# Performance work log

Measured on AMD Instinct MI355X. Metric: run time of the kernel, lower is better.

The kernel has to match this reference:

```python
import jax, jax.numpy as jnp
import numpy as np

_L, _DEPTH, _M, _NGEN, _C = 4, 7, 256, 8, 16


def _build_tree():
    # Complete _L-ary tree in BFS (level) order. t columns: [label, parent, position, child_0.._L-1]
    rng = np.random.default_rng(0)
    sizes = [_L ** d for d in range(_DEPTH + 1)]
    t_limits = np.concatenate([[0], np.cumsum(sizes)]).astype(np.int32)
    n = int(t_limits[-1])
    u = np.arange(n)
    parent = np.where(u > 0, (u - 1) // _L, 0)
    pos = np.where(u > 0, (u - 1) % _L, 0)
    labels = rng.integers(0, _M, n)
    ch = _L * u[:, None] + 1 + np.arange(_L)[None, :]
    ch = np.where(ch < n, ch, 0)  # 0 == no child (root is never a child)
    t = np.concatenate([labels[:, None], parent[:, None], pos[:, None], ch], axis=1).astype(np.int32)
    return t, t_limits


def setup_inputs():
    key = jax.random.key(0)
    ka, kb, kp = jax.random.split(key, 3)
    t, t_limits = _build_tree()
    return {
        'a': jax.random.normal(ka, (_NGEN, _C, _C, _L), jnp.float32),
        'b': jax.random.normal(kb, (_NGEN, _C, _M), jnp.float32),
        'pi': jax.random.normal(kp, (_NGEN, _C), jnp.float32),
        't': jnp.asarray(t),
        't_limits': jnp.asarray(t_limits),
    }


def _htmm_likelihood(a, b, pi, t, t_limits):
    t = np.asarray(t)
    lim = np.asarray(t_limits)
    n_levels = len(lim) - 1
    n = int(lim[-1])
    n_gen, C, _, L = a.shape
    sm_a = jax.nn.softmax(a, axis=1)    # [G, Ci(child), Cj(parent), L]
    sm_b = jax.nn.softmax(b, axis=2)    # [G, C, M]
    sm_pi = jax.nn.softmax(pi, axis=1)  # [G, C]

    # ---- preliminary downward: per-node state priors, level by level ----
    prior = jnp.zeros((n_gen, n, C), sm_pi.dtype).at[:, 0, :].set(sm_pi)
    for lev in range(1, n_levels):
        lo, hi = int(lim[lev]), int(lim[lev + 1])
        pos, pa = t[lo:hi, 2], t[lo:hi, 1]
        a_pos = sm_a[:, :, :, pos]                        # [G, Ci, Cj, nl]
        lev_prior = jnp.einsum('gijn,gnj->gni', a_pos, prior[:, pa, :])
        prior = prior.at[:, lo:hi, :].set(lev_prior)

    # ---- upward pass ----
    beta_i = jnp.zeros((n_gen, n, C), sm_pi.dtype)
    beta_il = jnp.zeros((n_gen, n + 1, C), sm_pi.dtype)   # extra dummy slot for padded children
    lo, hi = int(lim[-2]), int(lim[-1])                   # leaves
    em = sm_b[:, :, t[lo:hi, 0]].transpose(0, 2, 1)       # [G, n_leaf, C]
    bl = em * prior[:, lo:hi, :]
    beta_i = beta_i.at[:, lo:hi, :].set(bl / bl.sum(2, keepdims=True))
    a_t = sm_a.transpose(0, 3, 1, 2)                      # [G, L(pos), Ci, Cj]
    for lev in range(n_levels - 2, -1, -1):
        lo, hi = int(lim[lev]), int(lim[lev + 1])
        ch = t[lo:hi, 3:]                                 # [nl, L]
        mask = ch > 0
        safe = np.where(mask, ch, 0)
        ratio = beta_i[:, safe, :] / prior[:, safe, :]    # [G, nl, L, C]
        bil = jnp.einsum('gnlc,glcp->gnlp', ratio, a_t)   # [G, nl, L, Cj]
        aux = jnp.prod(jnp.where(mask[None, :, :, None], bil, 1.0), axis=2)
        em = sm_b[:, :, t[lo:hi, 0]].transpose(0, 2, 1)
        bi = aux * em * prior[:, lo:hi, :]
        beta_i = beta_i.at[:, lo:hi, :].set(bi / bi.sum(2, keepdims=True))
        scat = np.where(mask, ch, n).reshape(-1)          # padded children go to dummy slot
        beta_il = beta_il.at[:, scat, :].set(bil.reshape(n_gen, -1, C))
    beta_il = beta_il[:, :n, :].at[:, 0, :].set(0.0)

    # ---- downward pass: smoothed posteriors ----
    eps_i = jnp.zeros((n_gen, n, C), sm_pi.dtype).at[:, 0, :].set(beta_i[:, 0, :])
    eps_ijl = jnp.zeros((n_gen, n, C, C), sm_pi.dtype)
    for lev in range(1, n_levels):
        lo, hi = int(lim[lev]), int(lim[lev + 1])
        pos, pa = t[lo:hi, 2], t[lo:hi, 1]
        a_pos = sm_a[:, :, :, pos].transpose(0, 3, 1, 2)  # [G, nl, Ci, Cj]
        num = beta_i[:, lo:hi, :, None] * a_pos * eps_i[:, pa, None, :]
        den = prior[:, lo:hi, :, None] * beta_il[:, lo:hi, None, :]
        e_ijl = num / den
        e_i = e_ijl.sum(3)
        e_i = e_i / e_i.sum(2, keepdims=True)
        eps_i = eps_i.at[:, lo:hi, :].set(e_i)
        eps_ijl = eps_ijl.at[:, lo:hi, :, :].set(e_ijl)

    # ---- log-likelihood ----
    pi_lh = jnp.sum(eps_i[:, 0, :] * jnp.log(sm_pi), axis=-1)
    b_nodes = sm_b[:, :, t[:, 0]].transpose(0, 2, 1)      # [G, n, C]
    b_lh = jnp.sum(eps_i * jnp.log(b_nodes), axis=(1, 2))
    a_pos_all = sm_a[:, :, :, t[1:, 2]].transpose(0, 3, 1, 2)
    a_lh = jnp.sum(eps_ijl[:, 1:] * jnp.log(a_pos_all), axis=(1, 2, 3))
    return pi_lh + b_lh + a_lh  # [n_gen]


def reference(a, b, pi, t, t_limits):
    return _htmm_likelihood(a, b, pi, t, t_limits)
```

## Files before the change

### kernel.cpp

```cpp
#include <hip/hip_runtime.h>

#define NGEN 8
#define NC 16
#define NM 256
#define NNODE 21845

#define OFF_SMA_T  ((size_t)0)
#define OFF_SALA   ((size_t)8192)
#define OFF_SMA_U  ((size_t)16384)
#define OFF_SMB_T  ((size_t)24576)
#define OFF_LSMB_T ((size_t)57344)
#define OFF_SMPI   ((size_t)90112)
#define OFF_LSMPI  ((size_t)90240)
#define OFF_LAB    ((size_t)90368)
#define OFF_R4     ((size_t)112224)
#define OFF_EPS4   ((size_t)144992)
#define OFF_ST     ((size_t)177760)
#define ST_R7   0
#define ST_R6   1024
#define ST_R5   1280
#define ST_BIL7 1344
#define ST_BIL6 2368
#define ST_BIL5 2624
#define ST_SZ   2688

__device__ __forceinline__ float red16(float v) {
    v += __shfl_xor(v, 1, 16);
    v += __shfl_xor(v, 2, 16);
    v += __shfl_xor(v, 4, 16);
    v += __shfl_xor(v, 8, 16);
    return v;
}
__device__ __forceinline__ float rcpf(float x) { return __builtin_amdgcn_rcpf(x); }

__device__ __forceinline__ float dot16(const float* A, const float* row) {
    const float4* r4 = (const float4*)row;
    float s = 0.f;
#pragma unroll
    for (int q = 0; q < 4; ++q) {
        float4 t = r4[q];
        s += A[4 * q] * t.x + A[4 * q + 1] * t.y + A[4 * q + 2] * t.z + A[4 * q + 3] * t.w;
    }
    return s;
}
__device__ __forceinline__ void dot16x2(const float* A, const float* B, const float* row,
                                        float& s1, float& s2) {
    const float4* r4 = (const float4*)row;
#pragma unroll
    for (int q = 0; q < 4; ++q) {
        float4 t = r4[q];
        s1 += A[4 * q] * t.x + A[4 * q + 1] * t.y + A[4 * q + 2] * t.z + A[4 * q + 3] * t.w;
        s2 += B[4 * q] * t.x + B[4 * q + 1] * t.y + B[4 * q + 2] * t.z + B[4 * q + 3] * t.w;
    }
}

__device__ __forceinline__ void up_step4(const float (*Rch)[16], float (*BILch)[16],
                                         const float (*Ppar)[16], float (*Rpar)[16],
                                         const float* smb, int lab, int nd, int l, int p,
                                         const float* Aup) {
    int ch = 4 * nd + l;
    float bil = dot16(Aup, Rch[ch]);
    BILch[ch][p] = bil;
    float t0 = bil * __shfl_xor(bil, 16);
    float aux = t0 * __shfl_xor(t0, 32);
    float q0 = aux * smb[(size_t)lab * 16 + p];
    float bi = q0 * Ppar[nd][p];
    float ssum = red16(bi);
    if (l == 0) Rpar[nd][p] = q0 * rcpf(ssum);
}

__global__ __launch_bounds__(128) void k_init(const float* __restrict__ a,
                                              const float* __restrict__ b,
                                              const float* __restrict__ pi,
                                              const int* __restrict__ t,
                                              float* __restrict__ ws, float* __restrict__ out) {
    int bx = blockIdx.x, tid = threadIdx.x;
    if (bx < 128) {
        for (int k = bx * 128 + tid; k < NNODE; k += 128 * 128)
            ((int*)(ws + OFF_LAB))[k] = t[k * 7];
        if (tid < 64) {
            int g = bx >> 4, i = bx & 15;
            float v[4];
            float mx = -1e30f;
#pragma unroll
            for (int q = 0; q < 4; ++q) {
                v[q] = b[((size_t)(g * NC + i)) * NM + tid + 64 * q];
                mx = fmaxf(mx, v[q]);
            }
#pragma unroll
            for (int o = 1; o < 64; o <<= 1) mx = fmaxf(mx, __shfl_xor(mx, o));
            float e[4], s = 0.f;
#pragma unroll
            for (int q = 0; q < 4; ++q) { e[q] = expf(v[q] - mx); s += e[q]; }
#pragma unroll
            for (int o = 1; o < 64; o <<= 1) s += __shfl_xor(s, o);
            float ls = logf(s), rs = 1.0f / s;
#pragma unroll
            for (int q = 0; q < 4; ++q) {
                int m = tid + 64 * q;
                ws[OFF_SMB_T + ((size_t)g * NM + m) * NC + i] = e[q] * rs;
                ws[OFF_LSMB_T + ((size_t)g * NM + m) * NC + i] = v[q] - mx - ls;
            }
        }
        return;
    }
    int g = bx - 128;
    if (tid < 64) {
        int j = tid >> 2, l = tid & 3;
        size_t base = ((size_t)(g * NC) * NC + j) * 4 + l;
        float v[16];
        float mx = -1e30f;
#pragma unroll
        for (int i = 0; i < 16; ++i) { v[i] = a[base + (size_t)i * 64]; mx = fmaxf(mx, v[i]); }
        float e[16], s = 0.0f;
#pragma unroll
        for (int i = 0; i < 16; ++i) { e[i] = expf(v[i] - mx); s += e[i]; }
        float ls = logf(s), rs = 1.0f / s;
        size_t tb = ((size_t)(g * NC + j) * 4 + l) * NC;
#pragma unroll
        for (int i = 0; i < 16; ++i) {
            float sm = e[i] * rs;
            float lg = v[i] - mx - ls;
            ws[OFF_SMA_T + tb + i] = sm;
            ws[OFF_SALA + tb + i] = sm * lg;
            ws[OFF_SMA_U + ((size_t)(g * NC + i) * 4 + l) * NC + j] = sm;
        }
    } else if (tid == 64) {
        float v[16];
        float mx = -1e30f;
#pragma unroll
        for (int i = 0; i < 16; ++i) { v[i] = pi[g * NC + i]; mx = fmaxf(mx, v[i]); }
        float e[16], s = 0.0f;
#pragma unroll
        for (int i = 0; i < 16; ++i) { e[i] = expf(v[i] - mx); s += e[i]; }
        float ls = logf(s), rs = 1.0f / s;
#pragma unroll
        for (int i = 0; i < 16; ++i) {
            ws[OFF_SMPI + g * NC + i] = e[i] * rs;
            ws[OFF_LSMPI + g * NC + i] = v[i] - mx - ls;
        }
        out[g] = 0.0f;
    }
}

__global__ __launch_bounds__(256) void k_sub_up(float* __restrict__ ws) {
    int s = blockIdx.x, g = blockIdx.y, tid = threadIdx.x;
    int v = 85 + s;
    int i = tid & 15, grp = tid >> 4, pos = grp & 3;
    int lane = tid & 63, wv = tid >> 6;
    int l = lane >> 4, p = lane & 15;
    const float* sAg = ws + OFF_SMA_T + (size_t)g * 1024;
    const float* Aug = ws + OFF_SMA_U + (size_t)g * 1024;
    const float* smb = ws + OFF_SMB_T + (size_t)g * 4096;
    const int* LAB = (const int*)(ws + OFF_LAB);

    __shared__ __align__(16) float ST[ST_SZ];
    float (*R7)[16]   = (float(*)[16])(ST + ST_R7);
    float (*R6)[16]   = (float(*)[16])(ST + ST_R6);
    float (*R5)[16]   = (float(*)[16])(ST + ST_R5);
    float (*BIL7)[16] = (float(*)[16])(ST + ST_BIL7);
    float (*BIL6)[16] = (float(*)[16])(ST + ST_BIL6);
    float (*BIL5)[16] = (float(*)[16])(ST + ST_BIL5);
    __shared__ __align__(16) float P5[4][16], P6[16][16];
    __shared__ __align__(16) float P4[16];
    __shared__ int labs[85];

    if (tid < 64) labs[21 + tid] = LAB[64 * v + 21 + tid];
    else if (tid < 80) labs[5 + (tid - 64)] = LAB[16 * v + 5 + (tid - 64)];
    else if (tid < 84) labs[1 + (tid - 80)] = LAB[4 * v + 1 + (tid - 80)];
    else if (tid == 84) labs[0] = LAB[v];
    else if (tid >= 128 && tid < 144) {
        int v3 = (v - 1) >> 2, v2 = (v3 - 1) >> 2, v1 = (v2 - 1) >> 2;
        int chain[4] = {v1, v2, v3, v};
        float pr = ws[OFF_SMPI + g * 16 + i];
#pragma unroll
        for (int k = 0; k < 4; ++k) {
            int pk = (chain[k] - 1) & 3;
            float sacc = 0.f;
#pragma unroll
            for (int j = 0; j < 16; ++j) sacc += sAg[(j * 4 + pk) * 16 + i] * __shfl(pr, j, 16);
            pr = sacc;
        }
        P4[i] = pr;
    }
    float Areg[16];
#pragma unroll
    for (int j = 0; j < 16; ++j) Areg[j] = sAg[(j * 4 + pos) * 16 + i];
    __syncthreads();

    if (tid < 64) P5[grp][i] = dot16(Areg, P4);
    __syncthreads();
    P6[grp][i] = dot16(Areg, P5[grp >> 2]);
    __syncthreads();
#pragma unroll
    for (int k = 0; k < 4; ++k) {
        int nl = grp + 16 * k;
        float s7 = dot16(Areg, P6[nl >> 2]);
        float smbv = smb[(size_t)labs[21 + nl] * 16 + i];
        float bl = smbv * s7;
        float ssum = red16(bl);
        R7[nl][i] = smbv * rcpf(ssum);
    }
    __syncthreads();
    float Aup[16];
#pragma unroll
    for (int c = 0; c < 16; ++c) Aup[c] = Aug[(c * 4 + l) * 16 + p];
#pragma unroll
    for (int r = 0; r < 4; ++r)
        up_step4(R7, BIL7, P6, R6, smb, labs[5 + (wv + 4 * r)], wv + 4 * r, l, p, Aup);
    __syncthreads();
    up_step4(R6, BIL6, P5, R5, smb, labs[1 + wv], wv, l, p, Aup);
    __syncthreads();
    if (wv == 0) {
        float bil = dot16(Aup, R5[l]);
        BIL5[l][p] = bil;
        float t0 = bil * __shfl_xor(bil, 16);
        float aux = t0 * __shfl_xor(t0, 32);
        float q0 = aux * smb[(size_t)labs[0] * 16 + p];
        float bi = q0 * P4[p];
        float ssum = red16(bi);
        if (l == 0) ws[OFF_R4 + ((size_t)g * 256 + s) * 16 + p] = q0 * rcpf(ssum);
    }
    __syncthreads();
    float* dst = ws + OFF_ST + (size_t)(g * 256 + s) * ST_SZ;
#pragma unroll
    for (int k = tid; k < ST_SZ / 4; k += 256)
        ((float4*)dst)[k] = ((const float4*)ST)[k];
}

__global__ __launch_bounds__(1024) void k_top(float* __restrict__ ws, float* __restrict__ out) {
    int g = blockIdx.x, tid = threadIdx.x;
    int i = tid & 15, grp = tid >> 4, pos = grp & 3;
    int lane = tid & 63, wv = tid >> 6;
    int l = lane >> 4, p = lane & 15;
    const float* sAg = ws + OFF_SMA_T + (size_t)g * 1024;
    const float* sLg = ws + OFF_SALA + (size_t)g * 1024;
    const float* Aug = ws + OFF_SMA_U + (size_t)g * 1024;
    const float* smb = ws + OFF_SMB_T + (size_t)g * 4096;
    const float* lsmb = ws + OFF_LSMB_T + (size_t)g * 4096;
    const float* r4g = ws + OFF_R4 + (size_t)g * 4096;
    float* eps4 = ws + OFF_EPS4 + (size_t)g * 4096;
    const int* LAB = (const int*)(ws + OFF_LAB);

    __shared__ float Pt[85][16], Bt[85][16], BILt[341][16];
    __shared__ int labt[341];
    __shared__ float wsum[16];

    float Areg[16], Aup[16], sLreg[16];
#pragma unroll
    for (int j = 0; j < 16; ++j) {
        Areg[j] = sAg[(j * 4 + pos) * 16 + i];
        sLreg[j] = sLg[(j * 4 + pos) * 16 + i];
    }
#pragma unroll
    for (int c = 0; c < 16; ++c) Aup[c] = Aug[(c * 4 + l) * 16 + p];
    if (tid < 341) labt[tid] = LAB[tid];
    if (tid < 16) Pt[0][i] = ws[OFF_SMPI + g * 16 + i];
    __syncthreads();
    if (grp < 4) {
        float pv = Pt[0][i];
        float s = 0.f;
#pragma unroll
        for (int j = 0; j < 16; ++j) s += Areg[j] * __shfl(pv, j, 16);
        Pt[1 + grp][i] = s;
    }
    __syncthreads();
    if (grp < 16) {
        float pv = Pt[1 + (grp >> 2)][i];
        float s = 0.f;
#pragma unroll
        for (int j = 0; j < 16; ++j) s += Areg[j] * __shfl(pv, j, 16);
        Pt[5 + grp][i] = s;
    }
    __syncthreads();
    {
        float pv = Pt[5 + (grp >> 2)][i];
        float s = 0.f;
#pragma unroll
        for (int j = 0; j < 16; ++j) s += Areg[j] * __shfl(pv, j, 16);
        Pt[21 + grp][i] = s;
    }
    __syncthreads();
    for (int r = 0; r < 4; ++r) {
        int nd = wv + 16 * r;
        int chl = 4 * nd + l;
        float rv = r4g[(size_t)chl * 16 + p];
        float bil = 0.f;
#pragma unroll
        for (int c = 0; c < 16; ++c) bil += __shfl(rv, c, 16) * Aup[c];
        BILt[85 + chl][p] = bil;
        float t0 = bil * __shfl_xor(bil, 16);
        float aux = t0 * __shfl_xor(t0, 32);
        float bi = aux * smb[(size_t)labt[21 + nd] * 16 + p] * Pt[21 + nd][p];
        float ssum = red16(bi);
        if (l == 0) Bt[21 + nd][p] = bi * rcpf(ssum);
    }
    __syncthreads();
    {
        int nd = wv, ch = 21 + 4 * nd + l;
        float rv = Bt[ch][p] * rcpf(Pt[ch][p]);
        float bil = 0.f;
#pragma unroll
        for (int c = 0; c < 16; ++c) bil += __shfl(rv, c, 16) * Aup[c];
        BILt[ch][p] = bil;
        float t0 = bil * __shfl_xor(bil, 16);
        float aux = t0 * __shfl_xor(t0, 32);
        float bi = aux * smb[(size_t)labt[5 + nd] * 16 + p] * Pt[5 + nd][p];
        float ssum = red16(bi);
        if (l == 0) Bt[5 + nd][p] = bi * rcpf(ssum);
    }
    __syncthreads();
    if (wv < 4) {
        int nd = wv, ch = 5 + 4 * nd + l;
        float rv = Bt[ch][p] * rcpf(Pt[ch][p]);
        float bil = 0.f;
#pragma unroll
        for (int c = 0; c < 16; ++c) bil += __shfl(rv, c, 16) * Aup[c];
        BILt[ch][p] = bil;
        float t0 = bil * __shfl_xor(bil, 16);
        float aux = t0 * __shfl_xor(t0, 32);
        float bi = aux * smb[(size_t)labt[1 + nd] * 16 + p] * Pt[1 + nd][p];
        float ssum = red16(bi);
        if (l == 0) Bt[1 + nd][p] = bi * rcpf(ssum);
    }
    __syncthreads();
    if (wv == 0) {
        int ch = 1 + l;
        float rv = Bt[ch][p] * rcpf(Pt[ch][p]);
        float bil = 0.f;
#pragma unroll
        for (int c = 0; c < 16; ++c) bil += __shfl(rv, c, 16) * Aup[c];
        BILt[ch][p] = bil;
        float t0 = bil * __shfl_xor(bil, 16);
        float aux = t0 * __shfl_xor(t0, 32);
        float bi = aux * smb[(size_t)labt[0] * 16 + p] * Pt[0][p];
        float ssum = red16(bi);
        if (l == 0) Bt[0][p] = bi * rcpf(ssum);
    }
    __syncthreads();
    float acc = 0.f;
    if (tid < 16)
        acc += Bt[0][i] * (ws[OFF_LSMPI + g * 16 + i] + lsmb[(size_t)labt[0] * 16 + i]);
    if (grp < 4) {
        int row = 1 + grp;
        float w = Bt[0][i] * rcpf(BILt[row][i]);
        float c0 = Bt[row][i] * rcpf(Pt[row][i]);
        float s1 = 0.f, s2 = 0.f;
#pragma unroll
        for (int j = 0; j < 16; ++j) { float wj = __shfl(w, j, 16); s1 += Areg[j] * wj; s2 += sLreg[j] * wj; }
        float esum = c0 * s1, tot = red16(esum), ev = esum * rcpf(tot);
        Bt[row][i] = ev;
        acc += c0 * s2 + ev * lsmb[(size_t)labt[row] * 16 + i];
    }
    __syncthreads();
    if (grp < 16) {
        int row = 5 + grp, pa = 1 + (grp >> 2);
        float w = Bt[pa][i] * rcpf(BILt[row][i]);
        float c0 = Bt[row][i] * rcpf(Pt[row][i]);
        float s1 = 0.f, s2 = 0.f;
#pragma unroll
        for (int j = 0; j < 16; ++j) { float wj = __shfl(w, j, 16); s1 += Areg[j] * wj; s2 += sLreg[j] * wj; }
        float esum = c0 * s1, tot = red16(esum), ev = esum * rcpf(tot);
        Bt[row][i] = ev;
        acc += c0 * s2 + ev * lsmb[(size_t)labt[row] * 16 + i];
    }
    __syncthreads();
    {
        int row = 21 + grp, pa = 5 + (grp >> 2);
        float w = Bt[pa][i] * rcpf(BILt[row][i]);
        float c0 = Bt[row][i] * rcpf(Pt[row][i]);
        float s1 = 0.f, s2 = 0.f;
#pragma unroll
        for (int j = 0; j < 16; ++j) { float wj = __shfl(w, j, 16); s1 += Areg[j] * wj; s2 += sLreg[j] * wj; }
        float esum = c0 * s1, tot = red16(esum), ev = esum * rcpf(tot);
        Bt[row][i] = ev;
        acc += c0 * s2 + ev * lsmb[(size_t)labt[row] * 16 + i];
    }
    __syncthreads();
    for (int k = 0; k < 4; ++k) {
        int nl = grp + 64 * k;
        int row = 85 + nl, pa = 21 + (nl >> 2);
        float w = Bt[pa][i] * rcpf(BILt[row][i]);
        float c0 = r4g[(size_t)nl * 16 + i];
        float s1 = 0.f, s2 = 0.f;
#pragma unroll
        for (int j = 0; j < 16; ++j) { float wj = __shfl(w, j, 16); s1 += Areg[j] * wj; s2 += sLreg[j] * wj; }
        float esum = c0 * s1, tot = red16(esum), ev = esum * rcpf(tot);
        eps4[(size_t)nl * 16 + i] = ev;
        acc += c0 * s2 + ev * lsmb[(size_t)labt[row] * 16 + i];
    }
#pragma unroll
    for (int o = 1; o < 64; o <<= 1) acc += __shfl_xor(acc, o);
    if ((tid & 63) == 0) wsum[tid >> 6] = acc;
    __syncthreads();
    if (tid == 0) {
        float stot = 0.f;
#pragma unroll
        for (int w2 = 0; w2 < 16; ++w2) stot += wsum[w2];
        atomicAdd(&out[g], stot);
    }
}

__global__ __launch_bounds__(256) void k_sub_down(float* __restrict__ ws, float* __restrict__ out) {
    int s = blockIdx.x, g = blockIdx.y, tid = threadIdx.x;
    int v = 85 + s;
    int i = tid & 15, grp = tid >> 4, pos = grp & 3;
    const float* sAg = ws + OFF_SMA_T + (size_t)g * 1024;
    const float* sLg = ws + OFF_SALA + (size_t)g * 1024;
    const float* lsmb = ws + OFF_LSMB_T + (size_t)g * 4096;
    const int* LAB = (const int*)(ws + OFF_LAB);

    __shared__ __align__(16) float ST[ST_SZ];
    float (*R7)[16]   = (float(*)[16])(ST + ST_R7);
    float (*R6)[16]   = (float(*)[16])(ST + ST_R6);
    float (*R5)[16]   = (float(*)[16])(ST + ST_R5);
    float (*BIL7)[16] = (float(*)[16])(ST + ST_BIL7);
    float (*BIL6)[16] = (float(*)[16])(ST + ST_BIL6);
    float (*BIL5)[16] = (float(*)[16])(ST + ST_BIL5);
    __shared__ __align__(16) float E4[16];
    __shared__ int labs[85];
    __shared__ float wsum[4];

    const float* src = ws + OFF_ST + (size_t)(g * 256 + s) * ST_SZ;
#pragma unroll
    for (int k = tid; k < ST_SZ / 4; k += 256)
        ((float4*)ST)[k] = ((const float4*)src)[k];
    if (tid < 64) labs[21 + tid] = LAB[64 * v + 21 + tid];
    else if (tid < 80) labs[5 + (tid - 64)] = LAB[16 * v + 5 + (tid - 64)];
    else if (tid < 84) labs[1 + (tid - 80)] = LAB[4 * v + 1 + (tid - 80)];
    else if (tid == 84) labs[0] = LAB[v];
    else if (tid >= 96 && tid < 112) E4[tid - 96] = ws[OFF_EPS4 + ((size_t)g * 256 + s) * 16 + (tid - 96)];

    float Areg[16], sLreg[16];
#pragma unroll
    for (int j = 0; j < 16; ++j) {
        Areg[j] = sAg[(j * 4 + pos) * 16 + i];
        sLreg[j] = sLg[(j * 4 + pos) * 16 + i];
    }
    __syncthreads();

    float acc = 0.f;
    if (tid < 64) {
        float w = E4[i] * rcpf(BIL5[grp][i]);
        BIL5[grp][i] = w;
        float c0 = R5[grp][i];
        float s1 = 0.f, s2 = 0.f;
        dot16x2(Areg, sLreg, BIL5[grp], s1, s2);
        float esum = c0 * s1, tot = red16(esum), ev = esum * rcpf(tot);
        R5[grp][i] = ev;
        acc += c0 * s2 + ev * lsmb[(size_t)labs[1 + grp] * 16 + i];
    }
    __syncthreads();
    {
        float w = R5[grp >> 2][i] * rcpf(BIL6[grp][i]);
        BIL6[grp][i] = w;
        float c0 = R6[grp][i];
        float s1 = 0.f, s2 = 0.f;
        dot16x2(Areg, sLreg, BIL6[grp], s1, s2);
        float esum = c0 * s1, tot = red16(esum), ev = esum * rcpf(tot);
        R6[grp][i] = ev;
        acc += c0 * s2 + ev * lsmb[(size_t)labs[5 + grp] * 16 + i];
    }
    __syncthreads();
#pragma unroll
    for (int k = 0; k < 4; ++k) {
        int nl = grp + 16 * k;
        float w = R6[nl >> 2][i] * rcpf(BIL7[nl][i]);
        BIL7[nl][i] = w;
        float c0 = R7[nl][i];
        float s1 = 0.f, s2 = 0.f;
        dot16x2(Areg, sLreg, BIL7[nl], s1, s2);
        float esum = c0 * s1, tot = red16(esum), ev = esum * rcpf(tot);
        acc += c0 * s2 + ev * lsmb[(size_t)labs[21 + nl] * 16 + i];
    }
#pragma unroll
    for (int o = 1; o < 64; o <<= 1) acc += __shfl_xor(acc, o);
    if ((tid & 63) == 0) wsum[tid >> 6] = acc;
    __syncthreads();
    if (tid == 0) atomicAdd(&out[g], wsum[0] + wsum[1] + wsum[2] + wsum[3]);
}

extern "C" void kernel_launch(void* const* d_in, const int* in_sizes, int n_in,
                              void* d_out, int out_size, void* d_ws, size_t ws_size,
                              hipStream_t stream) {
    const float* a = (const float*)d_in[0];
    const float* b = (const float*)d_in[1];
    const float* pi = (const float*)d_in[2];
    const int* t = (const int*)d_in[3];
    float* out = (float*)d_out;
    float* ws = (float*)d_ws;

    k_init<<<136, 128, 0, stream>>>(a, b, pi, t, ws, out);
    k_sub_up<<<dim3(256, NGEN), 256, 0, stream>>>(ws);
    k_top<<<NGEN, 1024, 0, stream>>>(ws, out);
    k_sub_down<<<dim3(256, NGEN), 256, 0, stream>>>(ws, out);
}
```

Measured before the change: 76.08 us.

## Read labels directly from tree, use DPP reductions and LDS dot products

Drops the label-compaction pass in the init kernel and has each kernel read labels with a strided gather straight from the tree array. The 16-lane shuffle reductions become DPP row operations. In the top kernel, the shuffle-broadcast matrix-vector products are replaced by dot products that read vectors from shared memory, with the intermediate weights written back to LDS first. These changes trim instruction count and a global write/read pass, at the cost of uncoalesced strided label loads.

New measurement: 65.87 us. -13.4%, faster.

```diff
diff --git a/kernel.cpp b/kernel.cpp
--- a/kernel.cpp
+++ b/kernel.cpp
@@ -12,7 +12,6 @@
 #define OFF_LSMB_T ((size_t)57344)
 #define OFF_SMPI   ((size_t)90112)
 #define OFF_LSMPI  ((size_t)90240)
-#define OFF_LAB    ((size_t)90368)
 #define OFF_R4     ((size_t)112224)
 #define OFF_EPS4   ((size_t)144992)
 #define OFF_ST     ((size_t)177760)
@@ -24,11 +23,16 @@
 #define ST_BIL5 2624
 #define ST_SZ   2688
 
+template <int CTRL>
+__device__ __forceinline__ float dpp_row_add(float v) {
+    int s = __builtin_amdgcn_update_dpp(0, __float_as_int(v), CTRL, 0xf, 0xf, false);
+    return v + __int_as_float(s);
+}
 __device__ __forceinline__ float red16(float v) {
-    v += __shfl_xor(v, 1, 16);
-    v += __shfl_xor(v, 2, 16);
-    v += __shfl_xor(v, 4, 16);
-    v += __shfl_xor(v, 8, 16);
+    v = dpp_row_add<0x121>(v);
+    v = dpp_row_add<0x122>(v);
+    v = dpp_row_add<0x124>(v);
+    v = dpp_row_add<0x128>(v);
     return v;
 }
 __device__ __forceinline__ float rcpf(float x) { return __builtin_amdgcn_rcpf(x); }
@@ -72,12 +76,9 @@
 __global__ __launch_bounds__(128) void k_init(const float* __restrict__ a,
                                               const float* __restrict__ b,
                                               const float* __restrict__ pi,
-                                              const int* __restrict__ t,
                                               float* __restrict__ ws, float* __restrict__ out) {
     int bx = blockIdx.x, tid = threadIdx.x;
     if (bx < 128) {
-        for (int k = bx * 128 + tid; k < NNODE; k += 128 * 128)
-            ((int*)(ws + OFF_LAB))[k] = t[k * 7];
         if (tid < 64) {
             int g = bx >> 4, i = bx & 15;
             float v[4];
@@ -143,7 +144,7 @@
     }
 }
 
-__global__ __launch_bounds__(256) void k_sub_up(float* __restrict__ ws) {
+__global__ __launch_bounds__(256) void k_sub_up(float* __restrict__ ws, const int* __restrict__ t) {
     int s = blockIdx.x, g = blockIdx.y, tid = threadIdx.x;
     int v = 85 + s;
     int i = tid & 15, grp = tid >> 4, pos = grp & 3;
@@ -152,7 +153,6 @@
     const float* sAg = ws + OFF_SMA_T + (size_t)g * 1024;
     const float* Aug = ws + OFF_SMA_U + (size_t)g * 1024;
     const float* smb = ws + OFF_SMB_T + (size_t)g * 4096;
-    const int* LAB = (const int*)(ws + OFF_LAB);
 
     __shared__ __align__(16) float ST[ST_SZ];
     float (*R7)[16]   = (float(*)[16])(ST + ST_R7);
@@ -165,10 +165,10 @@
     __shared__ __align__(16) float P4[16];
     __shared__ int labs[85];
 
-    if (tid < 64) labs[21 + tid] = LAB[64 * v + 21 + tid];
-    else if (tid < 80) labs[5 + (tid - 64)] = LAB[16 * v + 5 + (tid - 64)];
-    else if (tid < 84) labs[1 + (tid - 80)] = LAB[4 * v + 1 + (tid - 80)];
-    else if (tid == 84) labs[0] = LAB[v];
+    if (tid < 64) labs[21 + tid] = t[(64 * v + 21 + tid) * 7];
+    else if (tid < 80) labs[5 + (tid - 64)] = t[(16 * v + 5 + (tid - 64)) * 7];
+    else if (tid < 84) labs[1 + (tid - 80)] = t[(4 * v + 1 + (tid - 80)) * 7];
+    else if (tid == 84) labs[0] = t[v * 7];
     else if (tid >= 128 && tid < 144) {
         int v3 = (v - 1) >> 2, v2 = (v3 - 1) >> 2, v1 = (v2 - 1) >> 2;
         int chain[4] = {v1, v2, v3, v};
@@ -228,7 +228,8 @@
         ((float4*)dst)[k] = ((const float4*)ST)[k];
 }
 
-__global__ __launch_bounds__(1024) void k_top(float* __restrict__ ws, float* __restrict__ out) {
+__global__ __launch_bounds__(1024) void k_top(float* __restrict__ ws, const int* __restrict__ t,
+                                              float* __restrict__ out) {
     int g = blockIdx.x, tid = threadIdx.x;
     int i = tid & 15, grp = tid >> 4, pos = grp & 3;
     int lane = tid & 63, wv = tid >> 6;
@@ -240,9 +241,8 @@
     const float* lsmb = ws + OFF_LSMB_T + (size_t)g * 4096;
     const float* r4g = ws + OFF_R4 + (size_t)g * 4096;
     float* eps4 = ws + OFF_EPS4 + (size_t)g * 4096;
-    const int* LAB = (const int*)(ws + OFF_LAB);
-
-    __shared__ float Pt[85][16], Bt[85][16], BILt[341][16];
+
+    __shared__ __align__(16) float Pt[85][16], Bt[85][16], BILt[341][16];
     __shared__ int labt[341];
     __shared__ float wsum[16];
 
@@ -254,32 +254,14 @@
     }
 #pragma unroll
     for (int c = 0; c < 16; ++c) Aup[c] = Aug[(c * 4 + l) * 16 + p];
-    if (tid < 341) labt[tid] = LAB[tid];
+    if (tid < 341) labt[tid] = t[tid * 7];
     if (tid < 16) Pt[0][i] = ws[OFF_SMPI + g * 16 + i];
     __syncthreads();
-    if (grp < 4) {
-        float pv = Pt[0][i];
-        float s = 0.f;
-#pragma unroll
-        for (int j = 0; j < 16; ++j) s += Areg[j] * __shfl(pv, j, 16);
-        Pt[1 + grp][i] = s;
-    }
-    __syncthreads();
-    if (grp < 16) {
-        float pv = Pt[1 + (grp >> 2)][i];
-        float s = 0.f;
-#pragma unroll
-        for (int j = 0; j < 16; ++j) s += Areg[j] * __shfl(pv, j, 16);
-        Pt[5 + grp][i] = s;
-    }
-    __syncthreads();
-    {
-        float pv = Pt[5 + (grp >> 2)][i];
-        float s = 0.f;
-#pragma unroll
-        for (int j = 0; j < 16; ++j) s += Areg[j] * __shfl(pv, j, 16);
-        Pt[21 + grp][i] = s;
-    }
+    if (grp < 4) Pt[1 + grp][i] = dot16(Areg, Pt[0]);
+    __syncthreads();
+    if (grp < 16) Pt[5 + grp][i] = dot16(Areg, Pt[1 + (grp >> 2)]);
+    __syncthreads();
+    Pt[21 + grp][i] = dot16(Areg, Pt[5 + (grp >> 2)]);
     __syncthreads();
     for (int r = 0; r < 4; ++r) {
         int nd = wv + 16 * r;
@@ -344,34 +326,34 @@
     if (grp < 4) {
         int row = 1 + grp;
         float w = Bt[0][i] * rcpf(BILt[row][i]);
+        BILt[row][i] = w;
         float c0 = Bt[row][i] * rcpf(Pt[row][i]);
         float s1 = 0.f, s2 = 0.f;
-#pragma unroll
-        for (int j = 0; j < 16; ++j) { float wj = __shfl(w, j, 16); s1 += Areg[j] * wj; s2 += sLreg[j] * wj; }
+        dot16x2(Areg, sLreg, BILt[row], s1, s2);
         float esum = c0 * s1, tot = red16(esum), ev = esum * rcpf(tot);
         Bt[row][i] = ev;
         acc += c0 * s2 + ev * lsmb[(size_t)labt[row] * 16 + i];
     }
     __syncthreads();
     if (grp < 16) {
-        int row = 5 + grp, pa = 1 + (grp >> 2);
-        float w = Bt[pa][i] * rcpf(BILt[row][i]);
+        int row = 5 + grp;
+        float w = Bt[1 + (grp >> 2)][i] * rcpf(BILt[row][i]);
+        BILt[row][i] = w;
         float c0 = Bt[row][i] * rcpf(Pt[row][i]);
         float s1 = 0.f, s2 = 0.f;
-#pragma unroll
-        for (int j = 0; j < 16; ++j) { float wj = __shfl(w, j, 16); s1 += Areg[j] * wj; s2 += sLreg[j] * wj; }
+        dot16x2(Areg, sLreg, BILt[row], s1, s2);
         float esum = c0 * s1, tot = red16(esum), ev = esum * rcpf(tot);
         Bt[row][i] = ev;
         acc += c0 * s2 + ev * lsmb[(size_t)labt[row] * 16 + i];
     }
     __syncthreads();
     {
-        int row = 21 + grp, pa = 5 + (grp >> 2);
-        float w = Bt[pa][i] * rcpf(BILt[row][i]);
+        int row = 21 + grp;
+        float w = Bt[5 + (grp >> 2)][i] * rcpf(BILt[row][i]);
+        BILt[row][i] = w;
         float c0 = Bt[row][i] * rcpf(Pt[row][i]);
         float s1 = 0.f, s2 = 0.f;
-#pragma unroll
-        for (int j = 0; j < 16; ++j) { float wj = __shfl(w, j, 16); s1 += Areg[j] * wj; s2 += sLreg[j] * wj; }
+        dot16x2(Areg, sLreg, BILt[row], s1, s2);
         float esum = c0 * s1, tot = red16(esum), ev = esum * rcpf(tot);
         Bt[row][i] = ev;
         acc += c0 * s2 + ev * lsmb[(size_t)labt[row] * 16 + i];
@@ -379,12 +361,12 @@
     __syncthreads();
     for (int k = 0; k < 4; ++k) {
         int nl = grp + 64 * k;
-        int row = 85 + nl, pa = 21 + (nl >> 2);
-        float w = Bt[pa][i] * rcpf(BILt[row][i]);
+        int row = 85 + nl;
+        float w = Bt[21 + (nl >> 2)][i] * rcpf(BILt[row][i]);
+        BILt[row][i] = w;
         float c0 = r4g[(size_t)nl * 16 + i];
         float s1 = 0.f, s2 = 0.f;
-#pragma unroll
-        for (int j = 0; j < 16; ++j) { float wj = __shfl(w, j, 16); s1 += Areg[j] * wj; s2 += sLreg[j] * wj; }
+        dot16x2(Areg, sLreg, BILt[row], s1, s2);
         float esum = c0 * s1, tot = red16(esum), ev = esum * rcpf(tot);
         eps4[(size_t)nl * 16 + i] = ev;
         acc += c0 * s2 + ev * lsmb[(size_t)labt[row] * 16 + i];
@@ -401,14 +383,14 @@
     }
 }
 
-__global__ __launch_bounds__(256) void k_sub_down(float* __restrict__ ws, float* __restrict__ out) {
+__global__ __launch_bounds__(256) void k_sub_down(float* __restrict__ ws, const int* __restrict__ t,
+                                                  float* __restrict__ out) {
     int s = blockIdx.x, g = blockIdx.y, tid = threadIdx.x;
     int v = 85 + s;
     int i = tid & 15, grp = tid >> 4, pos = grp & 3;
     const float* sAg = ws + OFF_SMA_T + (size_t)g * 1024;
     const float* sLg = ws + OFF_SALA + (size_t)g * 1024;
     const float* lsmb = ws + OFF_LSMB_T + (size_t)g * 4096;
-    const int* LAB = (const int*)(ws + OFF_LAB);
 
     __shared__ __align__(16) float ST[ST_SZ];
     float (*R7)[16]   = (float(*)[16])(ST + ST_R7);
@@ -425,10 +407,10 @@
 #pragma unroll
     for (int k = tid; k < ST_SZ / 4; k += 256)
         ((float4*)ST)[k] = ((const float4*)src)[k];
-    if (tid < 64) labs[21 + tid] = LAB[64 * v + 21 + tid];
-    else if (tid < 80) labs[5 + (tid - 64)] = LAB[16 * v + 5 + (tid - 64)];
-    else if (tid < 84) labs[1 + (tid - 80)] = LAB[4 * v + 1 + (tid - 80)];
-    else if (tid == 84) labs[0] = LAB[v];
+    if (tid < 64) labs[21 + tid] = t[(64 * v + 21 + tid) * 7];
+    else if (tid < 80) labs[5 + (tid - 64)] = t[(16 * v + 5 + (tid - 64)) * 7];
+    else if (tid < 84) labs[1 + (tid - 80)] = t[(4 * v + 1 + (tid - 80)) * 7];
+    else if (tid == 84) labs[0] = t[v * 7];
     else if (tid >= 96 && tid < 112) E4[tid - 96] = ws[OFF_EPS4 + ((size_t)g * 256 + s) * 16 + (tid - 96)];
 
     float Areg[16], sLreg[16];
@@ -490,8 +472,8 @@
     float* out = (float*)d_out;
     float* ws = (float*)d_ws;
 
-    k_init<<<136, 128, 0, stream>>>(a, b, pi, t, ws, out);
-    k_sub_up<<<dim3(256, NGEN), 256, 0, stream>>>(ws);
-    k_top<<<NGEN, 1024, 0, stream>>>(ws, out);
-    k_sub_down<<<dim3(256, NGEN), 256, 0, stream>>>(ws, out);
-}
+    k_init<<<136, 128, 0, stream>>>(a, b, pi, ws, out);
+    k_sub_up<<<dim3(256, NGEN), 256, 0, stream>>>(ws, t);
+    k_top<<<NGEN, 1024, 0, stream>>>(ws, t, out);
+    k_sub_down<<<dim3(256, NGEN), 256, 0, stream>>>(ws, t, out);
+}
```
